# Kernel optimization log

Measured on AMD Instinct MI355X. Metric: run time of the kernel, lower is better.

The kernel has to match this reference:

```python
import jax, jax.numpy as jnp
from jax import lax
import numpy as np

IMG = 800
SUB = 16
FS = IMG // SUB            # 50
NA = 9                     # 3 ratios x 3 scales
PRE_NMS = 6000             # test-mode n_test_pre_nms
POST_NMS = 300             # test-mode n_test_post_nms
NMS_THRESH = 0.7
MIN_BOX = 16.0
SLOPE = 0.01               # nn.LeakyReLU default


def build_anchors():
    # Faithful to _generate_anchor: x outer loop, y inner; ctr = grid - 8;
    # anchor rows are [x1, y1, w, h]; ratio outer, scale inner.
    c = np.arange(SUB, (FS + 1) * SUB, SUB).astype(np.float32) - 8.0  # 50 centers
    cx = np.repeat(c, FS)   # x is the outer loop
    cy = np.tile(c, FS)     # y is the inner loop
    rs = np.array([0.5, 1.0, 2.0], dtype=np.float32)
    ss = np.array([8.0, 16.0, 32.0], dtype=np.float32)
    hs = (SUB * ss[None, :] * np.sqrt(rs)[:, None]).reshape(-1)        # [9]
    ws = (SUB * ss[None, :] * np.sqrt(1.0 / rs)[:, None]).reshape(-1)  # [9]
    x1 = cx[:, None] - ws[None, :] / 2.0   # [2500, 9]
    y1 = cy[:, None] - hs[None, :] / 2.0
    w = np.broadcast_to(ws[None, :], x1.shape)
    h = np.broadcast_to(hs[None, :], x1.shape)
    return np.stack([x1, y1, w, h], axis=-1).reshape(-1, 4).astype(np.float32)  # [22500, 4]


def _conv(x, w, b, pad):
    y = lax.conv_general_dilated(x, w, (1, 1), ((pad, pad), (pad, pad)),
                                 dimension_numbers=("NCHW", "OIHW", "NCHW"))
    return y + b[None, :, None, None]


def _nms_keep(boxes):
    # Greedy NMS over score-sorted boxes [P,4] = (x1,y1,x2,y2); returns keep mask.
    x1, y1, x2, y2 = boxes[:, 0], boxes[:, 1], boxes[:, 2], boxes[:, 3]
    area = (x2 - x1 + 1.0) * (y2 - y1 + 1.0)
    P = boxes.shape[0]
    idx = jnp.arange(P)

    def body(i, keep):
        xx1 = jnp.maximum(x1[i], x1)
        yy1 = jnp.maximum(y1[i], y1)
        xx2 = jnp.minimum(x2[i], x2)
        yy2 = jnp.maximum(y2[i], y2)  # faithful to source bug: np.maximum, not minimum
        w = jnp.maximum(0.0, xx2 - xx1 + 1.0)
        h = jnp.maximum(0.0, yy2 - yy1 + 1.0)
        inter = w * h
        ov = inter / (area[i] + area - inter)
        suppress = (ov > NMS_THRESH) & (idx > i) & keep[i]
        return keep & ~suppress

    return lax.fori_loop(0, P, body, jnp.ones((P,), dtype=bool))


def _forward(in_features, conv_w, conv_b, reg_w, reg_b, cls_w, cls_b):
    B = in_features.shape[0]
    feat = _conv(in_features, conv_w, conv_b, 1)
    feat = jnp.where(feat >= 0, feat, SLOPE * feat)  # LeakyReLU(0.01)
    reg = _conv(feat, reg_w, reg_b, 0).transpose(0, 2, 3, 1).reshape(B, -1, 4)
    cls = _conv(feat, cls_w, cls_b, 0).transpose(0, 2, 3, 1).reshape(B, -1, 2)
    cls = jax.nn.softmax(cls, axis=2)

    anchors = jnp.asarray(build_anchors())  # [A,4] = (x1,y1,w,h)
    # The torch loop overwrites `rois` each batch iteration and returns only the
    # last batch's proposals; compute that directly.
    pr = reg[-1]                 # [A,4]
    score = cls[-1, :, 1]        # [A]
    hi = jnp.float32(IMG - 1)
    rx1 = jnp.clip(pr[:, 0] + anchors[:, 0], 0.0, hi)
    ry1 = jnp.clip(pr[:, 1] + anchors[:, 1], 0.0, hi)
    rx2 = jnp.clip(pr[:, 0] + anchors[:, 0] + pr[:, 2] + anchors[:, 2], 0.0, hi)
    ry2 = jnp.clip(pr[:, 1] + anchors[:, 1] + pr[:, 3] + anchors[:, 3], 0.0, hi)
    w = pr[:, 2] + anchors[:, 2]  # unclipped, as in source
    h = pr[:, 3] + anchors[:, 3]
    valid = (w >= MIN_BOX) & (h >= MIN_BOX)
    s = jnp.where(valid, score, -jnp.inf)   # filtered boxes sort to the end
    order = jnp.argsort(-s)[:PRE_NMS]       # top-6000 valid by objectness
    boxes = jnp.stack([rx1, ry1, rx2, ry2], axis=1)[order]  # [PRE,4]

    keep = _nms_keep(lax.stop_gradient(boxes))
    # first POST_NMS surviving boxes, in score order
    sel = jnp.argsort(jnp.where(keep, jnp.arange(PRE_NMS), PRE_NMS))[:POST_NMS]
    kb = boxes[sel]
    # output format: x1, y1, w, h
    return jnp.stack([kb[:, 0], kb[:, 1],
                      kb[:, 2] - kb[:, 0] + 1.0,
                      kb[:, 3] - kb[:, 1] + 1.0], axis=1)


def setup_inputs() -> dict:
    key = jax.random.key(0)
    k = jax.random.split(key, 4)
    return {
        "in_features": jax.random.normal(k[0], (8, 512, FS, FS), dtype=jnp.float32),
        "conv_w": jax.random.normal(k[1], (512, 512, 3, 3), dtype=jnp.float32) * 0.02,
        "conv_b": jnp.zeros((512,), dtype=jnp.float32),
        "reg_w": jax.random.normal(k[2], (36, 512, 1, 1), dtype=jnp.float32) * 0.02,
        "reg_b": jnp.zeros((36,), dtype=jnp.float32),
        "cls_w": jax.random.normal(k[3], (18, 512, 1, 1), dtype=jnp.float32) * 0.02,
        "cls_b": jnp.zeros((18,), dtype=jnp.float32),
    }


def reference(in_features, conv_w, conv_b, reg_w, reg_b, cls_w, cls_b):
    return _forward(in_features, conv_w, conv_b, reg_w, reg_b, cls_w, cls_b)
```

## Files before the change

### kernel.cpp

```cpp
#include <hip/hip_runtime.h>


#define NPIX 2500
#define NANCH 22500
#define NKEY 22528
#define PRE 6000
#define MASKW 94
#define MW 96
#define JCHUNK 1536
#define CS 8
#define KSLOT 8
#define PW 52
#define PSL 2704

__global__ __launch_bounds__(256) void prepK(
    const float* __restrict__ x,
    const float* __restrict__ wt,
    float* __restrict__ xpad,
    float* __restrict__ wtV)
{
    __shared__ float T[64][65];
    const int bx = blockIdx.x;
    if (bx < 512) {
        const int cin = bx;
        const float* src = x + (size_t)cin * NPIX;
        float* dst = xpad + (size_t)cin * PSL;
        for (int i = threadIdx.x; i < PSL; i += 256) {
            const int pr = i / PW;
            const int pc = i - pr * PW;
            float v = 0.f;
            if (pr >= 1 && pr <= 50 && pc >= 1 && pc <= 50)
                v = src[(pr - 1) * 50 + (pc - 1)];
            dst[i] = v;
        }
        return;
    }
    const int idx  = bx - 512;
    const int ct0  = (idx % 72) * 64;
    const int ocb  = (idx / 72) * 64;
    const int tid  = threadIdx.x;
    const int cidx = tid & 63;
    const int r4   = tid >> 6;
    #pragma unroll
    for (int i = 0; i < 16; ++i) {
        const int o = r4 + i * 4;
        T[o][cidx] = wt[(size_t)(ocb + o) * 4608 + ct0 + cidx];
    }
    __syncthreads();
    #pragma unroll
    for (int i = 0; i < 16; ++i) {
        const int ctl = ct0 + r4 + i * 4;
        const int cin = ctl / 9;
        const int t   = ctl - cin * 9;
        const int oc  = ocb + cidx;
        wtV[(((size_t)cin * 64 + (oc >> 3)) * 9 + t) * 8 + (oc & 7)] =
            T[cidx][r4 + i * 4];
    }
}

__global__ __launch_bounds__(256) void conv3x3_v9(
    const float* __restrict__ xpad,
    const float* __restrict__ wtV,
    float* __restrict__ part2)
{
    const int tid  = threadIdx.x;
    const int lane = tid & 63;
    const int wv   = tid >> 6;
    const int ocg  = blockIdx.x;
    const int pb   = blockIdx.y * 4 + wv;
    const int cing = blockIdx.z * 64;
    const int px0  = pb * 64 + lane;
    const int px1  = px0 + 1280;
    const bool act1 = (px1 < NPIX);
    const int r0 = px0 / 50, cc0 = px0 - r0 * 50;
    const int px1c = act1 ? px1 : 0;
    const int r1 = px1c / 50, cc1 = px1c - r1 * 50;

    const float* xb0 = xpad + (size_t)cing * PSL + (r0 + 1) * PW + (cc0 + 1);
    const float* xb1 = xpad + (size_t)cing * PSL + (r1 + 1) * PW + (cc1 + 1);

    float acc0[8], acc1[8];
    #pragma unroll
    for (int j = 0; j < 8; ++j) { acc0[j] = 0.f; acc1[j] = 0.f; }

    const float* wbase = wtV + ((size_t)cing * 64 + ocg) * 72;

    for (int cin = 0; cin < 64; ++cin) {
        float v0[9], v1[9];
        const float* xa = xb0 + (size_t)cin * PSL;
        const float* xc = xb1 + (size_t)cin * PSL;
        #pragma unroll
        for (int t = 0; t < 9; ++t) {
            const int dr = t / 3 - 1, dc = t % 3 - 1;
            v0[t] = xa[dr * PW + dc];
            v1[t] = xc[dr * PW + dc];
        }
        const float* wp = wbase + (size_t)cin * 4608;
        #pragma unroll
        for (int j = 0; j < 8; ++j) {
            float a = acc0[j];
            float b = acc1[j];
            #pragma unroll
            for (int t = 0; t < 9; ++t) {
                const float w = wp[t * 8 + j];
                a = fmaf(w, v0[t], a);
                b = fmaf(w, v1[t], b);
            }
            acc0[j] = a;
            acc1[j] = b;
        }
    }

    float* dst0 = part2 + ((size_t)blockIdx.z * 512 + ocg * 8) * NPIX + px0;
    #pragma unroll
    for (int j = 0; j < 8; ++j)
        dst0[(size_t)j * NPIX] = acc0[j];
    if (act1) {
        float* dst1 = part2 + ((size_t)blockIdx.z * 512 + ocg * 8) * NPIX + px1;
        #pragma unroll
        for (int j = 0; j < 8; ++j)
            dst1[(size_t)j * NPIX] = acc1[j];
    }
}

__global__ __launch_bounds__(256) void reduce_leaky4(
    const float* __restrict__ part2, const float* __restrict__ bias,
    float* __restrict__ feat)
{
    const int oc = blockIdx.x;
    const float b = bias[oc];
    float4* dstv = (float4*)(feat + (size_t)oc * NPIX);
    for (int q = threadIdx.x; q < 625; q += 256) {
        float4 s = make_float4(0.f, 0.f, 0.f, 0.f);
        #pragma unroll
        for (int k = 0; k < CS; ++k) {
            const float4 v = *(const float4*)(part2 + ((size_t)k * 512 + oc) * NPIX + q * 4);
            s.x += v.x; s.y += v.y; s.z += v.z; s.w += v.w;
        }
        s.x += b; s.y += b; s.z += b; s.w += b;
        s.x = (s.x >= 0.f) ? s.x : 0.01f * s.x;
        s.y = (s.y >= 0.f) ? s.y : 0.01f * s.y;
        s.z = (s.z >= 0.f) ? s.z : 0.01f * s.z;
        s.w = (s.w >= 0.f) ? s.w : 0.01f * s.w;
        dstv[q] = s;
    }
}

__global__ __launch_bounds__(256) void conv1x1_heads(
    const float* __restrict__ feat,
    const float* __restrict__ rw, const float* __restrict__ rb,
    const float* __restrict__ cw, const float* __restrict__ cb,
    float* __restrict__ regcls)
{
    __shared__ float sAcc[3][18][64];
    const int tid  = threadIdx.x;
    const int lane = tid & 63;
    const int wv   = tid >> 6;
    const int pix0 = blockIdx.x * 64 + lane;
    const bool act = (pix0 < NPIX);
    const int pix  = act ? pix0 : (NPIX - 1);
    const int chunk = blockIdx.y;
    const float* wb; const float* bb; int ocbase;
    if (chunk == 0)      { wb = rw;            bb = rb;      ocbase = 0;  }
    else if (chunk == 1) { wb = rw + 18 * 512; bb = rb + 18; ocbase = 18; }
    else                 { wb = cw;            bb = cb;      ocbase = 36; }

    float acc[18];
    #pragma unroll
    for (int k = 0; k < 18; ++k) acc[k] = 0.f;

    const int c0 = wv * 128;
    for (int cin = c0; cin < c0 + 128; ++cin) {
        const float v = feat[(size_t)cin * NPIX + pix];
        #pragma unroll
        for (int k = 0; k < 18; ++k)
            acc[k] = fmaf(wb[k * 512 + cin], v, acc[k]);
    }
    if (wv > 0) {
        #pragma unroll
        for (int k = 0; k < 18; ++k) sAcc[wv - 1][k][lane] = acc[k];
    }
    __syncthreads();
    if (wv == 0 && act) {
        #pragma unroll
        for (int k = 0; k < 18; ++k) {
            float s = acc[k];
            s += sAcc[0][k][lane];
            s += sAcc[1][k][lane];
            s += sAcc[2][k][lane];
            regcls[(size_t)(ocbase + k) * NPIX + pix] = s + bb[k];
        }
    }
}

__global__ __launch_bounds__(256) void decodeK(
    const float* __restrict__ regcls,
    float4* __restrict__ boxes,
    unsigned long long* __restrict__ keys)
{
    const int i = blockIdx.x * 256 + threadIdx.x;
    if (i >= NANCH) {
        if (i < NKEY) keys[i] = 0xFFFFFFFFFFFFFFFFull;
        return;
    }
    const int pos = i / 9;
    const int a   = i - pos * 9;
    const int hh  = pos / 50;
    const int wwp = pos - hh * 50;
    const int r = a / 3, s = a - r * 3;

    const float base_s[3] = {128.f, 256.f, 512.f};
    const float sq [3] = {0.70710678118654752440f, 1.0f, 1.41421356237309504880f};
    const float sqi[3] = {1.41421356237309504880f, 1.0f, 0.70710678118654752440f};
    const float hs = base_s[s] * sq[r];
    const float ws = base_s[s] * sqi[r];
    const float cx = (float)(hh * 16 + 8);
    const float cy = (float)(wwp * 16 + 8);
    const float ax = cx - ws * 0.5f;
    const float ay = cy - hs * 0.5f;

    const float pr0 = regcls[(size_t)(a * 4 + 0) * NPIX + pos];
    const float pr1 = regcls[(size_t)(a * 4 + 1) * NPIX + pos];
    const float pr2 = regcls[(size_t)(a * 4 + 2) * NPIX + pos];
    const float pr3 = regcls[(size_t)(a * 4 + 3) * NPIX + pos];
    const float c0  = regcls[(size_t)(36 + a * 2 + 0) * NPIX + pos];
    const float c1  = regcls[(size_t)(36 + a * 2 + 1) * NPIX + pos];

    const float m  = fmaxf(c0, c1);
    const float e0 = expf(c0 - m);
    const float e1 = expf(c1 - m);
    const float score = e1 / (e0 + e1);

    const float t0 = pr0 + ax;
    const float t1 = pr1 + ay;
    const float hi = 799.0f;
    const float rx1 = fminf(fmaxf(t0, 0.f), hi);
    const float ry1 = fminf(fmaxf(t1, 0.f), hi);
    const float rx2 = fminf(fmaxf((t0 + pr2) + ws, 0.f), hi);
    const float ry2 = fminf(fmaxf((t1 + pr3) + hs, 0.f), hi);
    const float bw = pr2 + ws;
    const float bh = pr3 + hs;
    const bool valid = (bw >= 16.f) && (bh >= 16.f);
    const float sc = valid ? score : -__builtin_inff();

    unsigned u = __float_as_uint(sc);
    u = (u & 0x80000000u) ? ~u : (u | 0x80000000u);
    const unsigned k32 = ~u;
    keys[i]  = ((unsigned long long)k32 << 32) | (unsigned)i;
    boxes[i] = make_float4(rx1, ry1, rx2, ry2);
}

__global__ __launch_bounds__(256) void rankK(
    const unsigned long long* __restrict__ keys, int* __restrict__ rank)
{
    const int i = blockIdx.x * 256 + threadIdx.x;
    const unsigned long long my = (i < NANCH) ? keys[i] : 0ull;
    const unsigned long long* kj = keys + blockIdx.y * 2816;
    int cnt = 0;
    for (int t = 0; t < 2816; t += 8) {
        #pragma unroll
        for (int q = 0; q < 8; ++q)
            cnt += (kj[t + q] < my) ? 1 : 0;
    }
    if (i < NANCH) atomicAdd(&rank[i], cnt);
}

__global__ __launch_bounds__(256) void scatterK(
    const float4* __restrict__ boxes, const int* __restrict__ rank,
    float4* __restrict__ sboxes)
{
    const int i = blockIdx.x * 256 + threadIdx.x;
    if (i < NANCH) {
        const int r = rank[i];
        if (r < PRE) sboxes[r] = boxes[i];
    }
}

__global__ __launch_bounds__(256) void nmsMaskK(
    const float4* __restrict__ sb, unsigned long long* __restrict__ mask)
{
    __shared__ float sx1[JCHUNK], sy1[JCHUNK], sx2[JCHUNK], sy2[JCHUNK], sar[JCHUNK];
    const int tid = threadIdx.x;
    const int jbase = blockIdx.y * JCHUNK;
    for (int t = tid; t < JCHUNK; t += 256) {
        const int j = jbase + t;
        if (j < PRE) {
            const float4 b = sb[j];
            sx1[t] = b.x; sy1[t] = b.y; sx2[t] = b.z; sy2[t] = b.w;
            sar[t] = (b.z - b.x + 1.f) * (b.w - b.y + 1.f);
        } else {
            sx1[t] = 0.f; sy1[t] = 0.f; sx2[t] = -1.f; sy2[t] = 0.f; sar[t] = 0.f;
        }
    }
    __syncthreads();
    const int i = blockIdx.x * 16 + (tid >> 4);
    const float4 bi = sb[i];
    const float x1 = bi.x, y1 = bi.y, x2 = bi.z, y2 = bi.w;
    const float ar = (x2 - x1 + 1.f) * (y2 - y1 + 1.f);
    for (int w = (tid & 15); w < 24; w += 16) {
        unsigned long long bits = 0ull;
        const int l0 = w * 64;
        for (int u = 0; u < 64; ++u) {
            const int j = jbase + l0 + u;
            if (j > i && j < PRE) {
                const int l = l0 + u;
                const float xx1 = fmaxf(x1, sx1[l]);
                const float yy1 = fmaxf(y1, sy1[l]);
                const float xx2 = fminf(x2, sx2[l]);
                const float yy2 = fmaxf(y2, sy2[l]);
                const float wv = fmaxf(0.f, xx2 - xx1 + 1.f);
                const float hv = fmaxf(0.f, yy2 - yy1 + 1.f);
                const float inter = wv * hv;
                const float ov = inter / ((ar + sar[l]) - inter);
                if (ov > 0.7f) bits |= (1ull << u);
            }
        }
        mask[(size_t)i * MW + blockIdx.y * 24 + w] = bits;
    }
}

__global__ __launch_bounds__(64) void nmsScanOutK(
    const unsigned long long* __restrict__ mask,
    const float4* __restrict__ sb,
    float* __restrict__ out)
{
    __shared__ int sKept[300];
    __shared__ unsigned long long sKeepW[MASKW];
    const int lane = threadIdx.x;

    unsigned long long rem0 = 0ull, rem1 = 0ull;
    int cnt = 0;
    int done = 0;

    unsigned long long d00 = mask[(size_t)lane * MW + 0];
    unsigned long long d01 = mask[(size_t)lane * MW + 1];
    unsigned long long d11 = mask[(size_t)(64 + lane) * MW + 1];

    for (int p = 0; p < 47 && !done; ++p) {
        const int g0 = 2 * p, g1 = 2 * p + 1;

        unsigned long long n00 = 0ull, n01 = 0ull, n11 = 0ull;
        if (p + 1 < 47) {
            const int h0 = g0 + 2, h1 = g0 + 3;
            const int ra = h0 * 64 + lane;
            const int rb = h1 * 64 + lane;
            n00 = mask[(size_t)ra * MW + h0];
            n01 = mask[(size_t)ra * MW + h1];
            if (rb < PRE) n11 = mask[(size_t)rb * MW + h1];
        }

        unsigned long long cur0, cur1;
        {
            unsigned lo, hi;
            if (g0 < 64) {
                lo = __builtin_amdgcn_readlane((unsigned)rem0, g0);
                hi = __builtin_amdgcn_readlane((unsigned)(rem0 >> 32), g0);
            } else {
                lo = __builtin_amdgcn_readlane((unsigned)rem1, g0 - 64);
                hi = __builtin_amdgcn_readlane((unsigned)(rem1 >> 32), g0 - 64);
            }
            cur0 = ((unsigned long long)hi << 32) | lo;
            if (g1 < 64) {
                lo = __builtin_amdgcn_readlane((unsigned)rem0, g1);
                hi = __builtin_amdgcn_readlane((unsigned)(rem0 >> 32), g1);
            } else {
                lo = __builtin_amdgcn_readlane((unsigned)rem1, g1 - 64);
                hi = __builtin_amdgcn_readlane((unsigned)(rem1 >> 32), g1 - 64);
            }
            cur1 = ((unsigned long long)hi << 32) | lo;
        }
        const unsigned long long valid0 = ~0ull;
        const unsigned long long valid1 =
            (g1 == MASKW - 1) ? 0x0000FFFFFFFFFFFFull : ~0ull;

        unsigned long long kb0 = 0ull, kb1 = 0ull;
        for (;;) {
            const unsigned long long nd = (~cur0) & valid0;
            if (!nd) break;
            const int b = __builtin_ctzll(nd);
            if (lane == 0 && cnt < 300) sKept[cnt] = g0 * 64 + b;
            ++cnt;
            kb0 |= (1ull << b);
            if (cnt >= 300) { done = 1; break; }
            const unsigned al = __builtin_amdgcn_readlane((unsigned)d00, b);
            const unsigned ah = __builtin_amdgcn_readlane((unsigned)(d00 >> 32), b);
            const unsigned bl = __builtin_amdgcn_readlane((unsigned)d01, b);
            const unsigned bh = __builtin_amdgcn_readlane((unsigned)(d01 >> 32), b);
            cur0 |= (1ull << b) | (((unsigned long long)ah << 32) | al);
            cur1 |= (((unsigned long long)bh << 32) | bl);
        }
        if (!done) {
            for (;;) {
                const unsigned long long nd = (~cur1) & valid1;
                if (!nd) break;
                const int b = __builtin_ctzll(nd);
                if (lane == 0 && cnt < 300) sKept[cnt] = g1 * 64 + b;
                ++cnt;
                kb1 |= (1ull << b);
                if (cnt >= 300) { done = 1; break; }
                const unsigned cl = __builtin_amdgcn_readlane((unsigned)d11, b);
                const unsigned ch = __builtin_amdgcn_readlane((unsigned)(d11 >> 32), b);
                cur1 |= (1ull << b) | (((unsigned long long)ch << 32) | cl);
            }
        }
        if (lane == 0) { sKeepW[g0] = kb0; sKeepW[g1] = kb1; }

        if (!done && (kb0 | kb1)) {
            unsigned long long a0 = 0ull, a1 = 0ull;
            {
                int kbit[KSLOT];
                unsigned long long t = kb0;
                #pragma unroll
                for (int s = 0; s < KSLOT; ++s) {
                    kbit[s] = t ? __builtin_ctzll(t) : 64;
                    t &= t - 1;
                }
                #pragma unroll
                for (int s = 0; s < KSLOT; ++s) {
                    if (kbit[s] < 64) {
                        const unsigned long long* pr =
                            mask + (size_t)(g0 * 64 + kbit[s]) * MW;
                        a0 |= pr[lane];
                        a1 |= (lane < MASKW - 64) ? pr[64 + lane] : 0ull;
                    }
                }
                while (t) {
                    const int b = __builtin_ctzll(t); t &= t - 1;
                    const unsigned long long* pr =
                        mask + (size_t)(g0 * 64 + b) * MW;
                    a0 |= pr[lane];
                    a1 |= (lane < MASKW - 64) ? pr[64 + lane] : 0ull;
                }
            }
            {
                int kbit[KSLOT];
                unsigned long long t = kb1;
                #pragma unroll
                for (int s = 0; s < KSLOT; ++s) {
                    kbit[s] = t ? __builtin_ctzll(t) : 64;
                    t &= t - 1;
                }
                #pragma unroll
                for (int s = 0; s < KSLOT; ++s) {
                    if (kbit[s] < 64) {
                        const unsigned long long* pr =
                            mask + (size_t)(g1 * 64 + kbit[s]) * MW;
                        a0 |= pr[lane];
                        a1 |= (lane < MASKW - 64) ? pr[64 + lane] : 0ull;
                    }
                }
                while (t) {
                    const int b = __builtin_ctzll(t); t &= t - 1;
                    const unsigned long long* pr =
                        mask + (size_t)(g1 * 64 + b) * MW;
                    a0 |= pr[lane];
                    a1 |= (lane < MASKW - 64) ? pr[64 + lane] : 0ull;
                }
            }
            rem0 |= a0;
            rem1 |= a1;
        }
        d00 = n00; d01 = n01; d11 = n11;
    }

    __syncthreads();

    if (cnt < 300) {
        int c = cnt;
        for (int g = 0; g < MASKW && c < 300; ++g) {
            const unsigned long long valid =
                (g == MASKW - 1) ? 0x0000FFFFFFFFFFFFull : ~0ull;
            unsigned long long u = (~sKeepW[g]) & valid;
            while (u && c < 300) {
                const int b = __builtin_ctzll(u); u &= u - 1;
                if (lane == 0) sKept[c] = g * 64 + b;
                ++c;
            }
        }
    }
    __syncthreads();

    for (int s = lane; s < 300; s += 64) {
        const float4 b = sb[sKept[s]];
        out[s * 4 + 0] = b.x;
        out[s * 4 + 1] = b.y;
        out[s * 4 + 2] = b.z - b.x + 1.0f;
        out[s * 4 + 3] = b.w - b.y + 1.0f;
    }
}

extern "C" void kernel_launch(void* const* d_in, const int* in_sizes, int n_in,
                              void* d_out, int out_size, void* d_ws, size_t ws_size,
                              hipStream_t stream)
{
    (void)in_sizes; (void)n_in; (void)out_size; (void)ws_size;
    const float* x   = (const float*)d_in[0] + (size_t)7 * 512 * NPIX;
    const float* cw3 = (const float*)d_in[1];
    const float* cb3 = (const float*)d_in[2];
    const float* rw  = (const float*)d_in[3];
    const float* rb  = (const float*)d_in[4];
    const float* clw = (const float*)d_in[5];
    const float* clb = (const float*)d_in[6];
    float* out = (float*)d_out;

    char* p = (char*)d_ws;
    auto alloc = [&](size_t n) { char* r = p; p += (n + 255) & ~(size_t)255; return r; };
    float*  part2  = (float*)alloc((size_t)CS * 512 * NPIX * 4);
    float*  wtV    = (float*)alloc((size_t)4608 * 512 * 4);
    float*  xpad   = (float*)alloc((size_t)512 * PSL * 4);
    float*  feat   = (float*)alloc((size_t)512 * NPIX * 4);
    float*  regcls = (float*)alloc((size_t)54 * NPIX * 4);
    float4* boxes  = (float4*)alloc((size_t)NANCH * 16);
    unsigned long long* keys = (unsigned long long*)alloc((size_t)NKEY * 8);
    int*    rank   = (int*)alloc((size_t)NANCH * 4);
    float4* sboxes = (float4*)alloc((size_t)PRE * 16);
    unsigned long long* mask = (unsigned long long*)alloc((size_t)PRE * MW * 8);

    hipMemsetAsync(rank, 0, (size_t)NANCH * 4, stream);
    prepK         <<<1088, 256, 0, stream>>>(x, cw3, xpad, wtV);
    conv3x3_v9    <<<dim3(64, 5, CS), 256, 0, stream>>>(xpad, wtV, part2);
    reduce_leaky4 <<<512, 256, 0, stream>>>(part2, cb3, feat);
    conv1x1_heads <<<dim3(40, 3), 256, 0, stream>>>(feat, rw, rb, clw, clb, regcls);
    decodeK       <<<88, 256, 0, stream>>>(regcls, boxes, keys);
    rankK         <<<dim3(88, 8), 256, 0, stream>>>(keys, rank);
    scatterK      <<<88, 256, 0, stream>>>(boxes, rank, sboxes);
    nmsMaskK      <<<dim3(375, 4), 256, 0, stream>>>(sboxes, mask);
    nmsScanOutK   <<<1, 64, 0, stream>>>(mask, sboxes, out);
}
```

Measured before the change: 573.9 us.

## Rebuild NMS mask kernel with lane-per-box wavefront ballots

The NMS overlap-mask kernel no longer stages j-boxes in shared memory or loops serially over 64 candidates per thread. Each wavefront lane now loads one j-box from global memory and tests it against 4 i-boxes held in registers, building each 64-bit mask word with __ballot. This removes the serial inner loop, the LDS staging and the block barrier. In exchange it adds one lane-0 store per word and relies on cache hits for the repeated sb reads.

```diff
diff --git a/kernel.cpp b/kernel.cpp
--- a/kernel.cpp
+++ b/kernel.cpp
@@ -279,43 +279,41 @@
 __global__ __launch_bounds__(256) void nmsMaskK(
     const float4* __restrict__ sb, unsigned long long* __restrict__ mask)
 {
-    __shared__ float sx1[JCHUNK], sy1[JCHUNK], sx2[JCHUNK], sy2[JCHUNK], sar[JCHUNK];
-    const int tid = threadIdx.x;
+    const int tid  = threadIdx.x;
+    const int lane = tid & 63;
+    const int wv   = tid >> 6;
+    const int i0   = blockIdx.x * 16 + wv * 4;
     const int jbase = blockIdx.y * JCHUNK;
-    for (int t = tid; t < JCHUNK; t += 256) {
-        const int j = jbase + t;
-        if (j < PRE) {
-            const float4 b = sb[j];
-            sx1[t] = b.x; sy1[t] = b.y; sx2[t] = b.z; sy2[t] = b.w;
-            sar[t] = (b.z - b.x + 1.f) * (b.w - b.y + 1.f);
-        } else {
-            sx1[t] = 0.f; sy1[t] = 0.f; sx2[t] = -1.f; sy2[t] = 0.f; sar[t] = 0.f;
-        }
-    }
-    __syncthreads();
-    const int i = blockIdx.x * 16 + (tid >> 4);
-    const float4 bi = sb[i];
-    const float x1 = bi.x, y1 = bi.y, x2 = bi.z, y2 = bi.w;
-    const float ar = (x2 - x1 + 1.f) * (y2 - y1 + 1.f);
-    for (int w = (tid & 15); w < 24; w += 16) {
-        unsigned long long bits = 0ull;
-        const int l0 = w * 64;
-        for (int u = 0; u < 64; ++u) {
-            const int j = jbase + l0 + u;
-            if (j > i && j < PRE) {
-                const int l = l0 + u;
-                const float xx1 = fmaxf(x1, sx1[l]);
-                const float yy1 = fmaxf(y1, sy1[l]);
-                const float xx2 = fminf(x2, sx2[l]);
-                const float yy2 = fmaxf(y2, sy2[l]);
-                const float wv = fmaxf(0.f, xx2 - xx1 + 1.f);
-                const float hv = fmaxf(0.f, yy2 - yy1 + 1.f);
-                const float inter = wv * hv;
-                const float ov = inter / ((ar + sar[l]) - inter);
-                if (ov > 0.7f) bits |= (1ull << u);
-            }
-        }
-        mask[(size_t)i * MW + blockIdx.y * 24 + w] = bits;
+
+    float ix1[4], iy1[4], ix2[4], iy2[4], iar[4];
+    #pragma unroll
+    for (int ii = 0; ii < 4; ++ii) {
+        const float4 b = sb[i0 + ii];
+        ix1[ii] = b.x; iy1[ii] = b.y; ix2[ii] = b.z; iy2[ii] = b.w;
+        iar[ii] = (b.z - b.x + 1.f) * (b.w - b.y + 1.f);
+    }
+
+    for (int w = 0; w < 24; ++w) {
+        const int j  = jbase + w * 64 + lane;
+        const int jc = (j < PRE) ? j : 0;
+        const float4 bj = sb[jc];
+        const float jar = (bj.z - bj.x + 1.f) * (bj.w - bj.y + 1.f);
+        #pragma unroll
+        for (int ii = 0; ii < 4; ++ii) {
+            const int i = i0 + ii;
+            const float xx1 = fmaxf(ix1[ii], bj.x);
+            const float yy1 = fmaxf(iy1[ii], bj.y);
+            const float xx2 = fminf(ix2[ii], bj.z);
+            const float yy2 = fmaxf(iy2[ii], bj.w);
+            const float wvv = fmaxf(0.f, xx2 - xx1 + 1.f);
+            const float hvv = fmaxf(0.f, yy2 - yy1 + 1.f);
+            const float inter = wvv * hvv;
+            const float ov = inter / ((iar[ii] + jar) - inter);
+            const bool pred = (j > i) && (j < PRE) && (ov > 0.7f);
+            const unsigned long long bits = __ballot(pred);
+            if (lane == 0)
+                mask[(size_t)i * MW + blockIdx.y * 24 + w] = bits;
+        }
     }
 }
 
```

New measurement: 501.7 us. 1.14x faster.
